# Performance work log

Measured on AMD Instinct MI355X. Metric: run time of the kernel, lower is better.

## Reference

```python
import jax, jax.numpy as jnp
import numpy as np

C1 = 256
C2 = 256
C = 256

def setup_inputs() -> dict:
    key = jax.random.key(0)
    ks = jax.random.split(key, 8)
    B, S, H, W = 4, 8, 32, 32
    img_feat = jax.random.normal(ks[0], (B, S, C1, H, W), dtype=jnp.float32)
    depth_feat = jax.random.normal(ks[1], (B, S, C2, H, W), dtype=jnp.float32)
    sq = 1.0 / np.sqrt(C1)
    sk = 1.0 / np.sqrt(C2)
    Wq = jax.random.uniform(ks[2], (C1, C), jnp.float32, -sq, sq)
    bq = jax.random.uniform(ks[3], (C,), jnp.float32, -sq, sq)
    Wk = jax.random.uniform(ks[4], (C2, C), jnp.float32, -sk, sk)
    bk = jax.random.uniform(ks[5], (C,), jnp.float32, -sk, sk)
    Wv = jax.random.uniform(ks[6], (C2, C), jnp.float32, -sk, sk)
    bv = jax.random.uniform(ks[7], (C,), jnp.float32, -sk, sk)
    return {"img_feat": img_feat, "depth_feat": depth_feat,
            "Wq": Wq, "bq": bq, "Wk": Wk, "bk": bk, "Wv": Wv, "bv": bv}

def reference(img_feat, depth_feat, Wq, bq, Wk, bk, Wv, bv):
    B, S, _, H, W = img_feat.shape
    hw = H * W
    # channels-last, flatten spatial: [B,S,hw,c1]
    img = jnp.transpose(img_feat, (0, 1, 3, 4, 2)).reshape(B, S, hw, -1)
    depth = jnp.transpose(depth_feat, (0, 1, 3, 4, 2)).reshape(B, S, hw, -1)
    q = (img @ Wq + bq).astype(jnp.float32)    # [B,S,hw,c]
    k = (depth @ Wk + bk).astype(jnp.float32)  # [B,S,hw,c]
    v = (depth @ Wv + bv).astype(jnp.float32)  # [B,S,hw,c]
    scale = 1.0 / jnp.sqrt(jnp.float32(Wq.shape[1]))
    scores = jnp.einsum('bsqc,bskc->bsqk', q, k) * scale  # [B,S,hw,hw]
    attn = jax.nn.softmax(scores, axis=-1)
    out = jnp.einsum('bsqk,bskc->bsqc', attn, v)          # [B,S,hw,c]
    out = out + img                                        # residual (c == c1)
    out = out.reshape(B, S, H, W, -1).astype(img_feat.dtype)
    return jnp.transpose(out, (0, 1, 4, 2, 3))             # [B,S,c,H,W]
```

## Files before the change

### kernel.cpp

```cpp
#include <hip/hip_runtime.h>
#include <hip/hip_bf16.h>

typedef __hip_bfloat16 bf16;
typedef __attribute__((ext_vector_type(8))) short short8v;
typedef __attribute__((ext_vector_type(4))) float f32x4;

#define NSLICE 32
#define HW     1024
#define CDIM   256
#define KVT    32
#define NKT    (HW / KVT)

#define FLASH_LDS_BYTES ((32768 + 2048) * 2)

__global__ __launch_bounds__(256)
void wt_prep_kernel(const float* __restrict__ Wq, const float* __restrict__ Wk,
                    const float* __restrict__ Wv, bf16* __restrict__ wt)
{
    const int m = blockIdx.x >> 8;
    const int r = blockIdx.x & 255;
    const int tid = threadIdx.x;
    const float* W = (m == 0) ? Wq : (m == 1) ? Wk : Wv;
    const float sc = (m == 0) ? 0.0625f : 1.0f;
    wt[((size_t)m << 16) + (size_t)tid * 256 + r] = __float2bfloat16(W[r * 256 + tid] * sc);
}

__global__ __launch_bounds__(256)
void proj_q_kernel(const float* __restrict__ img, const bf16* __restrict__ wt,
                   const float* __restrict__ bq, bf16* __restrict__ qo)
{
    const int bid   = blockIdx.x;
    const int s     = (bid & 7) * 4 + ((bid >> 3) & 3);
    const int tt    = (bid >> 5) & 15;
    const int chalf = bid >> 9;
    const int t0    = tt * 64;

    const int tid  = threadIdx.x;
    const int wave = tid >> 6;
    const int lane = tid & 63;
    const int lo16 = lane & 15;
    const int hi4  = lane >> 4;
    const int cw0  = chalf * 128 + wave * 32;

    __shared__ short Ai[64][40];

    const int so = tid >> 6, st = tid & 63;
    const float* imgS = img + (size_t)s * CDIM * HW + t0;

    f32x4 aq[2][4];
    #pragma unroll
    for (int a = 0; a < 2; ++a)
        #pragma unroll
        for (int b = 0; b < 4; ++b) aq[a][b] = (f32x4){0.f, 0.f, 0.f, 0.f};

    float ri[8];
    #pragma unroll
    for (int j = 0; j < 8; ++j) ri[j] = imgS[(size_t)(so * 8 + j) * HW + st];

    for (int kc = 0; kc < 8; ++kc) {
        __syncthreads();
        {
            short ti[8];
            #pragma unroll
            for (int j = 0; j < 8; ++j) {
                bf16 hb = __float2bfloat16(ri[j]);
                ti[j] = *reinterpret_cast<short*>(&hb);
            }
            *reinterpret_cast<short8v*>(&Ai[st][so * 8]) = *reinterpret_cast<short8v*>(ti);
        }
        __syncthreads();

        if (kc < 7) {
            #pragma unroll
            for (int j = 0; j < 8; ++j)
                ri[j] = imgS[(size_t)((kc + 1) * 32 + so * 8 + j) * HW + st];
        }

        short8v xi[4];
        #pragma unroll
        for (int nf = 0; nf < 4; ++nf)
            xi[nf] = *reinterpret_cast<const short8v*>(&Ai[nf * 16 + lo16][hi4 * 8]);

        const int koff = kc * 32 + hi4 * 8;
        short8v wqf[2];
        #pragma unroll
        for (int mf = 0; mf < 2; ++mf)
            wqf[mf] = *reinterpret_cast<const short8v*>(
                wt + (size_t)(cw0 + mf * 16 + lo16) * 256 + koff);

        #pragma unroll
        for (int mf = 0; mf < 2; ++mf)
            #pragma unroll
            for (int nf = 0; nf < 4; ++nf)
                aq[mf][nf] = __builtin_amdgcn_mfma_f32_16x16x32_bf16(wqf[mf], xi[nf], aq[mf][nf], 0, 0, 0);
    }

    #pragma unroll
    for (int mf = 0; mf < 2; ++mf) {
        const int cb = cw0 + mf * 16 + 4 * hi4;
        const float4 b4 = *reinterpret_cast<const float4*>(bq + cb);
        const float ba[4] = {b4.x * 0.0625f, b4.y * 0.0625f, b4.z * 0.0625f, b4.w * 0.0625f};
        #pragma unroll
        for (int nf = 0; nf < 4; ++nf) {
            const int tok = t0 + nf * 16 + lo16;
            bf16 tq[4];
            #pragma unroll
            for (int g = 0; g < 4; ++g)
                tq[g] = __float2bfloat16(aq[mf][nf][g] + ba[g]);
            *reinterpret_cast<uint2*>(&qo[((size_t)s * HW + tok) * CDIM + cb]) =
                *reinterpret_cast<uint2*>(tq);
        }
    }
}

__global__ __launch_bounds__(256)
void proj_kv_kernel(const float* __restrict__ dep, const bf16* __restrict__ wt,
                    const float* __restrict__ bk, const float* __restrict__ bv,
                    bf16* __restrict__ ko, bf16* __restrict__ vt)
{
    const int bid   = blockIdx.x;
    const int s     = (bid & 7) * 4 + ((bid >> 3) & 3);
    const int tt    = (bid >> 5) & 15;
    const int chalf = bid >> 9;
    const int t0    = tt * 64;

    const int tid  = threadIdx.x;
    const int wave = tid >> 6;
    const int lane = tid & 63;
    const int lo16 = lane & 15;
    const int hi4  = lane >> 4;
    const int cw0  = chalf * 128 + wave * 32;

    __shared__ short Ad[64][40];

    const int so = tid >> 6, st = tid & 63;
    const float* depS = dep + (size_t)s * CDIM * HW + t0;
    const bf16* wtk = wt + (1 << 16);
    const bf16* wtv = wt + (2 << 16);

    f32x4 ak[2][4], av[4][2];
    #pragma unroll
    for (int a = 0; a < 2; ++a)
        #pragma unroll
        for (int b = 0; b < 4; ++b) {
            ak[a][b] = (f32x4){0.f, 0.f, 0.f, 0.f};
            av[b][a] = (f32x4){0.f, 0.f, 0.f, 0.f};
        }

    float rd[8];
    #pragma unroll
    for (int j = 0; j < 8; ++j) rd[j] = depS[(size_t)(so * 8 + j) * HW + st];

    for (int kc = 0; kc < 8; ++kc) {
        __syncthreads();
        {
            short td[8];
            #pragma unroll
            for (int j = 0; j < 8; ++j) {
                bf16 hb = __float2bfloat16(rd[j]);
                td[j] = *reinterpret_cast<short*>(&hb);
            }
            *reinterpret_cast<short8v*>(&Ad[st][so * 8]) = *reinterpret_cast<short8v*>(td);
        }
        __syncthreads();

        if (kc < 7) {
            #pragma unroll
            for (int j = 0; j < 8; ++j)
                rd[j] = depS[(size_t)((kc + 1) * 32 + so * 8 + j) * HW + st];
        }

        short8v xd[4];
        #pragma unroll
        for (int nf = 0; nf < 4; ++nf)
            xd[nf] = *reinterpret_cast<const short8v*>(&Ad[nf * 16 + lo16][hi4 * 8]);

        const int koff = kc * 32 + hi4 * 8;
        short8v wkf[2], wvf[2];
        #pragma unroll
        for (int mf = 0; mf < 2; ++mf) {
            const size_t wrow = (size_t)(cw0 + mf * 16 + lo16) * 256 + koff;
            wkf[mf] = *reinterpret_cast<const short8v*>(wtk + wrow);
            wvf[mf] = *reinterpret_cast<const short8v*>(wtv + wrow);
        }

        #pragma unroll
        for (int mf = 0; mf < 2; ++mf)
            #pragma unroll
            for (int nf = 0; nf < 4; ++nf)
                ak[mf][nf] = __builtin_amdgcn_mfma_f32_16x16x32_bf16(wkf[mf], xd[nf], ak[mf][nf], 0, 0, 0);
        #pragma unroll
        for (int mf = 0; mf < 4; ++mf)
            #pragma unroll
            for (int nf = 0; nf < 2; ++nf)
                av[mf][nf] = __builtin_amdgcn_mfma_f32_16x16x32_bf16(xd[mf], wvf[nf], av[mf][nf], 0, 0, 0);
    }

    #pragma unroll
    for (int mf = 0; mf < 2; ++mf) {
        const int cb = cw0 + mf * 16 + 4 * hi4;
        const float4 b4 = *reinterpret_cast<const float4*>(bk + cb);
        const float ba[4] = {b4.x, b4.y, b4.z, b4.w};
        #pragma unroll
        for (int nf = 0; nf < 4; ++nf) {
            const int tok = t0 + nf * 16 + lo16;
            bf16 tk[4];
            #pragma unroll
            for (int g = 0; g < 4; ++g)
                tk[g] = __float2bfloat16(ak[mf][nf][g] + ba[g]);
            *reinterpret_cast<uint2*>(&ko[((size_t)s * HW + tok) * CDIM + cb]) =
                *reinterpret_cast<uint2*>(tk);
        }
    }
    #pragma unroll
    for (int nf = 0; nf < 2; ++nf) {
        const int c = cw0 + nf * 16 + lo16;
        const float bvv = bv[c];
        #pragma unroll
        for (int mf = 0; mf < 4; ++mf) {
            const int tb = t0 + mf * 16 + 4 * hi4;
            bf16 tv[4];
            #pragma unroll
            for (int g = 0; g < 4; ++g)
                tv[g] = __float2bfloat16(av[mf][nf][g] + bvv);
            *reinterpret_cast<uint2*>(&vt[((size_t)s * CDIM + c) * HW + tb]) =
                *reinterpret_cast<uint2*>(tv);
        }
    }
}

__global__ __launch_bounds__(256)
void flash_mfma_kernel(const bf16* __restrict__ q, const bf16* __restrict__ k,
                       const bf16* __restrict__ vt, const float* __restrict__ img,
                       float* __restrict__ out)
{
    const int bid = blockIdx.x;
    const int s   = (bid & 7) * 4 + ((bid >> 3) & 3);
    const int t0  = (bid >> 5) * 64;

    const int tid  = threadIdx.x;
    const int wave = tid >> 6;
    const int lane = tid & 63;
    const int lo16 = lane & 15;
    const int hi4  = lane >> 4;

    extern __shared__ short SM[];

    short8v qf[8];
    {
        const bf16* qp = q + ((size_t)s * HW + t0 + wave * 16 + lo16) * CDIM + hi4 * 8;
        #pragma unroll
        for (int kf = 0; kf < 8; ++kf)
            qf[kf] = *reinterpret_cast<const short8v*>(qp + kf * 32);
    }

    f32x4 Oacc[16];
    #pragma unroll
    for (int cf = 0; cf < 16; ++cf) Oacc[cf] = (f32x4){0.f, 0.f, 0.f, 0.f};
    float lp[4] = {0.f, 0.f, 0.f, 0.f};

    const bf16* kS  = k  + (size_t)s * HW * CDIM;
    const bf16* vtS = vt + (size_t)s * CDIM * HW;

    const int krow = tid >> 3;
    const int kch  = tid & 7;
    const int kxor = krow & 7;
    const int vxor = (tid >> 1) & 3;

    short8v kreg[4], vreg[4];
    #pragma unroll
    for (int u = 0; u < 4; ++u) {
        kreg[u] = *reinterpret_cast<const short8v*>(kS + (size_t)krow * CDIM + (kch + 8 * u) * 8);
        vreg[u] = *reinterpret_cast<const short8v*>(vtS + (size_t)tid * HW + u * 8);
    }

    #pragma unroll
    for (int u = 0; u < 4; ++u)
        *reinterpret_cast<short8v*>(&SM[krow * 256 + ((kch ^ kxor) + 8 * u) * 8]) = kreg[u];
    #pragma unroll
    for (int u = 0; u < 4; ++u)
        *reinterpret_cast<short8v*>(&SM[16384 + tid * 32 + (u ^ vxor) * 8]) = vreg[u];
    __syncthreads();

    const int pvRow = lo16 * 32 + (hi4 ^ ((lo16 >> 1) & 3)) * 8;
    for (int kt = 0; kt < NKT; ++kt) {
        const int cur = kt & 1;
        const int nxt = cur ^ 1;
        short* Kc = SM + cur * 8192;
        short* Vc = SM + 16384 + cur * 8192;

        if (kt + 1 < NKT) {
            const bf16* src = kS + (size_t)(kt + 1) * KVT * CDIM;
            #pragma unroll
            for (int u = 0; u < 4; ++u) {
                kreg[u] = *reinterpret_cast<const short8v*>(src + (size_t)krow * CDIM + (kch + 8 * u) * 8);
                vreg[u] = *reinterpret_cast<const short8v*>(vtS + (size_t)tid * HW + (kt + 1) * KVT + u * 8);
            }
        }

        f32x4 sa[2];
        sa[0] = (f32x4){0.f, 0.f, 0.f, 0.f};
        sa[1] = (f32x4){0.f, 0.f, 0.f, 0.f};
        __builtin_amdgcn_s_setprio(1);
        #pragma unroll
        for (int ks = 0; ks < 8; ++ks) {
            #pragma unroll
            for (int cf = 0; cf < 2; ++cf) {
                const int row = cf * 16 + lo16;
                short8v bfr = *reinterpret_cast<const short8v*>(
                    &Kc[row * 256 + ((4 * ks + hi4) ^ (lo16 & 7)) * 8]);
                sa[cf] = __builtin_amdgcn_mfma_f32_16x16x32_bf16(qf[ks], bfr, sa[cf], 0, 0, 0);
            }
        }
        __builtin_amdgcn_s_setprio(0);

        #pragma unroll
        for (int cf = 0; cf < 2; ++cf)
            #pragma unroll
            for (int g = 0; g < 4; ++g) {
                const float e = __expf(sa[cf][g]);
                lp[g] += e;
                bf16 hb = __float2bfloat16(e);
                const int r = 4 * hi4 + g;
                const int ch = (2 * cf + (lo16 >> 3)) ^ ((r >> 1) & 3);
                SM[32768 + wave * 512 + r * 32 + ch * 8 + (lo16 & 7)] = *reinterpret_cast<short*>(&hb);
            }

        const short8v pa = *reinterpret_cast<const short8v*>(&SM[32768 + wave * 512 + pvRow]);

        __builtin_amdgcn_s_setprio(1);
        #pragma unroll
        for (int cf = 0; cf < 16; ++cf) {
            const int row = cf * 16 + lo16;
            const short8v vb = *reinterpret_cast<const short8v*>(
                &Vc[row * 32 + (hi4 ^ ((lo16 >> 1) & 3)) * 8]);
            Oacc[cf] = __builtin_amdgcn_mfma_f32_16x16x32_bf16(pa, vb, Oacc[cf], 0, 0, 0);
        }
        __builtin_amdgcn_s_setprio(0);

        if (kt + 1 < NKT) {
            short* Kn = SM + nxt * 8192;
            short* Vn = SM + 16384 + nxt * 8192;
            #pragma unroll
            for (int u = 0; u < 4; ++u)
                *reinterpret_cast<short8v*>(&Kn[krow * 256 + ((kch ^ kxor) + 8 * u) * 8]) = kreg[u];
            #pragma unroll
            for (int u = 0; u < 4; ++u)
                *reinterpret_cast<short8v*>(&Vn[tid * 32 + (u ^ vxor) * 8]) = vreg[u];
        }
        __syncthreads();
    }

    float inv[4];
    #pragma unroll
    for (int g = 0; g < 4; ++g) {
        float l = lp[g];
        #pragma unroll
        for (int off = 1; off < 16; off <<= 1) l += __shfl_xor(l, off);
        inv[g] = 1.0f / l;
    }
    const float* imgS = img + (size_t)s * CDIM * HW;
    float*       outS = out + (size_t)s * CDIM * HW;
    const int tt = t0 + wave * 16 + 4 * hi4;
    #pragma unroll
    for (int cf = 0; cf < 16; ++cf) {
        const int c = cf * 16 + lo16;
        const float4 r4 = *reinterpret_cast<const float4*>(imgS + (size_t)c * HW + tt);
        float4 o;
        o.x = Oacc[cf][0] * inv[0] + r4.x;
        o.y = Oacc[cf][1] * inv[1] + r4.y;
        o.z = Oacc[cf][2] * inv[2] + r4.z;
        o.w = Oacc[cf][3] * inv[3] + r4.w;
        *reinterpret_cast<float4*>(outS + (size_t)c * HW + tt) = o;
    }
}

extern "C" void kernel_launch(void* const* d_in, const int* in_sizes, int n_in,
                              void* d_out, int out_size, void* d_ws, size_t ws_size,
                              hipStream_t stream)
{
    const float* img = (const float*)d_in[0];
    const float* dep = (const float*)d_in[1];
    const float* Wq  = (const float*)d_in[2];
    const float* bq  = (const float*)d_in[3];
    const float* Wk  = (const float*)d_in[4];
    const float* bk  = (const float*)d_in[5];
    const float* Wv  = (const float*)d_in[6];
    const float* bv  = (const float*)d_in[7];
    float* out = (float*)d_out;

    const size_t npt  = (size_t)NSLICE * HW * CDIM;
    const size_t need = 3 * npt * sizeof(bf16) + 3 * 65536 * sizeof(bf16);
    if (ws_size < need) {
        hipMemsetAsync(d_out, 0, (size_t)out_size * sizeof(float), stream);
        return;
    }

    bf16* q  = (bf16*)d_ws;
    bf16* k  = q + npt;
    bf16* vt = k + npt;
    bf16* wt = vt + npt;

    hipFuncSetAttribute((const void*)flash_mfma_kernel,
                        hipFuncAttributeMaxDynamicSharedMemorySize,
                        FLASH_LDS_BYTES);

    wt_prep_kernel<<<dim3(3 * 256), 256, 0, stream>>>(Wq, Wk, Wv, wt);

    proj_q_kernel<<<dim3(NSLICE * 32), 256, 0, stream>>>(img, wt, bq, q);
    proj_kv_kernel<<<dim3(NSLICE * 32), 256, 0, stream>>>(dep, wt, bk, bv, k, vt);

    flash_mfma_kernel<<<dim3(NSLICE * 16), 256, FLASH_LDS_BYTES, stream>>>(
        q, k, vt, img, out);
}
```

Baseline: 122.7 us.

## Stage full activation tile in swizzled LDS before projection MFMA loop

Q and KV projection kernels now load and convert the whole 64x256 activation tile into shared memory up front, with an XOR swizzle to avoid bank conflicts. The per-chunk double sync and register prefetch are replaced by a single barrier before a fully unrolled MFMA loop. This issues all global loads at once to get more memory-level parallelism and removes 16 barriers per block. The cost is a 32KB LDS footprint per block, which may reduce occupancy, and no overlap between loading and compute.

```diff
diff --git a/kernel.cpp b/kernel.cpp
--- a/kernel.cpp
+++ b/kernel.cpp
@@ -42,45 +42,43 @@
     const int hi4  = lane >> 4;
     const int cw0  = chalf * 128 + wave * 32;
 
-    __shared__ short Ai[64][40];
+    __shared__ short A[64 * 256];
 
     const int so = tid >> 6, st = tid & 63;
     const float* imgS = img + (size_t)s * CDIM * HW + t0;
 
+    #pragma unroll
+    for (int kc = 0; kc < 8; ++kc) {
+        float r[8];
+        #pragma unroll
+        for (int j = 0; j < 8; ++j)
+            r[j] = imgS[(size_t)(kc * 32 + so * 8 + j) * HW + st];
+        short tw[8];
+        #pragma unroll
+        for (int j = 0; j < 8; ++j) {
+            bf16 hb = __float2bfloat16(r[j]);
+            tw[j] = *reinterpret_cast<short*>(&hb);
+        }
+        const int ch = (kc * 4 + so) ^ (st & 7);
+        *reinterpret_cast<short8v*>(&A[st * 256 + ch * 8]) = *reinterpret_cast<short8v*>(tw);
+    }
+    __syncthreads();
+
     f32x4 aq[2][4];
     #pragma unroll
     for (int a = 0; a < 2; ++a)
         #pragma unroll
         for (int b = 0; b < 4; ++b) aq[a][b] = (f32x4){0.f, 0.f, 0.f, 0.f};
 
-    float ri[8];
-    #pragma unroll
-    for (int j = 0; j < 8; ++j) ri[j] = imgS[(size_t)(so * 8 + j) * HW + st];
-
+    #pragma unroll
     for (int kc = 0; kc < 8; ++kc) {
-        __syncthreads();
-        {
-            short ti[8];
-            #pragma unroll
-            for (int j = 0; j < 8; ++j) {
-                bf16 hb = __float2bfloat16(ri[j]);
-                ti[j] = *reinterpret_cast<short*>(&hb);
-            }
-            *reinterpret_cast<short8v*>(&Ai[st][so * 8]) = *reinterpret_cast<short8v*>(ti);
-        }
-        __syncthreads();
-
-        if (kc < 7) {
-            #pragma unroll
-            for (int j = 0; j < 8; ++j)
-                ri[j] = imgS[(size_t)((kc + 1) * 32 + so * 8 + j) * HW + st];
-        }
-
         short8v xi[4];
         #pragma unroll
-        for (int nf = 0; nf < 4; ++nf)
-            xi[nf] = *reinterpret_cast<const short8v*>(&Ai[nf * 16 + lo16][hi4 * 8]);
-
+        for (int nf = 0; nf < 4; ++nf) {
+            const int r  = nf * 16 + lo16;
+            const int ch = (kc * 4 + hi4) ^ (lo16 & 7);
+            xi[nf] = *reinterpret_cast<const short8v*>(&A[r * 256 + ch * 8]);
+        }
         const int koff = kc * 32 + hi4 * 8;
         short8v wqf[2];
         #pragma unroll
@@ -131,13 +129,30 @@
     const int hi4  = lane >> 4;
     const int cw0  = chalf * 128 + wave * 32;
 
-    __shared__ short Ad[64][40];
+    __shared__ short A[64 * 256];
 
     const int so = tid >> 6, st = tid & 63;
     const float* depS = dep + (size_t)s * CDIM * HW + t0;
     const bf16* wtk = wt + (1 << 16);
     const bf16* wtv = wt + (2 << 16);
 
+    #pragma unroll
+    for (int kc = 0; kc < 8; ++kc) {
+        float r[8];
+        #pragma unroll
+        for (int j = 0; j < 8; ++j)
+            r[j] = depS[(size_t)(kc * 32 + so * 8 + j) * HW + st];
+        short tw[8];
+        #pragma unroll
+        for (int j = 0; j < 8; ++j) {
+            bf16 hb = __float2bfloat16(r[j]);
+            tw[j] = *reinterpret_cast<short*>(&hb);
+        }
+        const int ch = (kc * 4 + so) ^ (st & 7);
+        *reinterpret_cast<short8v*>(&A[st * 256 + ch * 8]) = *reinterpret_cast<short8v*>(tw);
+    }
+    __syncthreads();
+
     f32x4 ak[2][4], av[4][2];
     #pragma unroll
     for (int a = 0; a < 2; ++a)
@@ -147,34 +162,15 @@
             av[b][a] = (f32x4){0.f, 0.f, 0.f, 0.f};
         }
 
-    float rd[8];
-    #pragma unroll
-    for (int j = 0; j < 8; ++j) rd[j] = depS[(size_t)(so * 8 + j) * HW + st];
-
+    #pragma unroll
     for (int kc = 0; kc < 8; ++kc) {
-        __syncthreads();
-        {
-            short td[8];
-            #pragma unroll
-            for (int j = 0; j < 8; ++j) {
-                bf16 hb = __float2bfloat16(rd[j]);
-                td[j] = *reinterpret_cast<short*>(&hb);
-            }
-            *reinterpret_cast<short8v*>(&Ad[st][so * 8]) = *reinterpret_cast<short8v*>(td);
-        }
-        __syncthreads();
-
-        if (kc < 7) {
-            #pragma unroll
-            for (int j = 0; j < 8; ++j)
-                rd[j] = depS[(size_t)((kc + 1) * 32 + so * 8 + j) * HW + st];
-        }
-
         short8v xd[4];
         #pragma unroll
-        for (int nf = 0; nf < 4; ++nf)
-            xd[nf] = *reinterpret_cast<const short8v*>(&Ad[nf * 16 + lo16][hi4 * 8]);
-
+        for (int nf = 0; nf < 4; ++nf) {
+            const int r  = nf * 16 + lo16;
+            const int ch = (kc * 4 + hi4) ^ (lo16 & 7);
+            xd[nf] = *reinterpret_cast<const short8v*>(&A[r * 256 + ch * 8]);
+        }
         const int koff = kc * 32 + hi4 * 8;
         short8v wkf[2], wvf[2];
         #pragma unroll
```

New measurement: 127.9 us. +4.2%, slower.

## Stage K/V tiles with direct global-to-LDS loads instead of register staging

Applied to the files above, without the earlier changes.

Replaces the register-staged double-buffer prefetch of K and V tiles with global_load_lds direct-to-LDS transfers. It also changes the V tile's LDS layout to chunk-major and moves the K swizzle into the global source address. This removes the register pressure and the VALU/LDS store instructions of the old staging path. The risk is that the async loads are only fenced by the end-of-iteration syncthreads (vmcnt wait), which could expose load latency. The new V layout may also cause LDS bank conflicts.

```diff
diff --git a/kernel.cpp b/kernel.cpp
--- a/kernel.cpp
+++ b/kernel.cpp
@@ -12,6 +12,13 @@
 #define NKT    (HW / KVT)
 
 #define FLASH_LDS_BYTES ((32768 + 2048) * 2)
+
+__device__ __forceinline__ void gl_lds16(const void* g, void* l) {
+    __builtin_amdgcn_global_load_lds(
+        (const __attribute__((address_space(1))) unsigned int*)g,
+        (__attribute__((address_space(3))) unsigned int*)l,
+        16, 0, 0);
+}
 
 __global__ __launch_bounds__(256)
 void wt_prep_kernel(const float* __restrict__ Wq, const float* __restrict__ Wk,
@@ -262,41 +269,35 @@
     const bf16* kS  = k  + (size_t)s * HW * CDIM;
     const bf16* vtS = vt + (size_t)s * CDIM * HW;
 
-    const int krow = tid >> 3;
-    const int kch  = tid & 7;
-    const int kxor = krow & 7;
-    const int vxor = (tid >> 1) & 3;
-
-    short8v kreg[4], vreg[4];
-    #pragma unroll
-    for (int u = 0; u < 4; ++u) {
-        kreg[u] = *reinterpret_cast<const short8v*>(kS + (size_t)krow * CDIM + (kch + 8 * u) * 8);
-        vreg[u] = *reinterpret_cast<const short8v*>(vtS + (size_t)tid * HW + u * 8);
-    }
-
-    #pragma unroll
-    for (int u = 0; u < 4; ++u)
-        *reinterpret_cast<short8v*>(&SM[krow * 256 + ((kch ^ kxor) + 8 * u) * 8]) = kreg[u];
-    #pragma unroll
-    for (int u = 0; u < 4; ++u)
-        *reinterpret_cast<short8v*>(&SM[16384 + tid * 32 + (u ^ vxor) * 8]) = vreg[u];
+    auto stage = [&](int kt_, int buf) {
+        short* Kb = SM + buf * 8192;
+        short* Vb = SM + 16384 + buf * 8192;
+        #pragma unroll
+        for (int u = 0; u < 4; ++u) {
+            const int i   = wave * 4 + u;
+            const int row = 2 * i + (lane >> 5);
+            const int ch  = (lane & 31) ^ (row & 7);
+            gl_lds16(kS + (size_t)(kt_ * KVT + row) * CDIM + ch * 8,
+                     Kb + i * 512);
+        }
+        #pragma unroll
+        for (int u = 0; u < 4; ++u) {
+            const int c = wave * 64 + lane;
+            gl_lds16(vtS + (size_t)c * HW + kt_ * KVT + u * 8,
+                     Vb + u * 2048 + wave * 512);
+        }
+    };
+
+    stage(0, 0);
     __syncthreads();
 
     const int pvRow = lo16 * 32 + (hi4 ^ ((lo16 >> 1) & 3)) * 8;
     for (int kt = 0; kt < NKT; ++kt) {
         const int cur = kt & 1;
-        const int nxt = cur ^ 1;
         short* Kc = SM + cur * 8192;
         short* Vc = SM + 16384 + cur * 8192;
 
-        if (kt + 1 < NKT) {
-            const bf16* src = kS + (size_t)(kt + 1) * KVT * CDIM;
-            #pragma unroll
-            for (int u = 0; u < 4; ++u) {
-                kreg[u] = *reinterpret_cast<const short8v*>(src + (size_t)krow * CDIM + (kch + 8 * u) * 8);
-                vreg[u] = *reinterpret_cast<const short8v*>(vtS + (size_t)tid * HW + (kt + 1) * KVT + u * 8);
-            }
-        }
+        if (kt + 1 < NKT) stage(kt + 1, cur ^ 1);
 
         f32x4 sa[2];
         sa[0] = (f32x4){0.f, 0.f, 0.f, 0.f};
@@ -331,23 +332,12 @@
         __builtin_amdgcn_s_setprio(1);
         #pragma unroll
         for (int cf = 0; cf < 16; ++cf) {
-            const int row = cf * 16 + lo16;
             const short8v vb = *reinterpret_cast<const short8v*>(
-                &Vc[row * 32 + (hi4 ^ ((lo16 >> 1) & 3)) * 8]);
+                &Vc[hi4 * 2048 + (cf * 16 + lo16) * 8]);
             Oacc[cf] = __builtin_amdgcn_mfma_f32_16x16x32_bf16(pa, vb, Oacc[cf], 0, 0, 0);
         }
         __builtin_amdgcn_s_setprio(0);
 
-        if (kt + 1 < NKT) {
-            short* Kn = SM + nxt * 8192;
-            short* Vn = SM + 16384 + nxt * 8192;
-            #pragma unroll
-            for (int u = 0; u < 4; ++u)
-                *reinterpret_cast<short8v*>(&Kn[krow * 256 + ((kch ^ kxor) + 8 * u) * 8]) = kreg[u];
-            #pragma unroll
-            for (int u = 0; u < 4; ++u)
-                *reinterpret_cast<short8v*>(&Vn[tid * 32 + (u ^ vxor) * 8]) = vreg[u];
-        }
         __syncthreads();
     }
 
```

New measurement: 120.8 us. No clear change (-1.6%).
